# Performance work log

Measured on AMD Instinct MI355X. Metric: run time of the kernel, lower is better.

Reference implementation:

```python
import jax, jax.numpy as jnp
import numpy as np

BATCH = 32
N_LEVELS = (16384, 4096, 1024, 256)   # nodes at each mesh resolution
M_LEVELS = (4096, 1024, 256, 64)      # nodes after each Pool (downsample)
DEG = 6                               # directed edges per node
POOL_K = 3                            # nnz per row of downsample matrix
FILTERS = (3, 32, 32, 32, 64)         # channel chain of the 4 ChebConvs
K_CHEB = 6                            # Chebyshev polynomial order


def setup_inputs() -> dict:
    key = jax.random.key(0)
    ks = iter(jax.random.split(key, 64))
    inp = {"x": jax.random.normal(next(ks), (BATCH, N_LEVELS[0], FILTERS[0]), jnp.float32)}
    for i, N in enumerate(N_LEVELS):
        er = jnp.repeat(jnp.arange(N), DEG)
        off = jax.random.randint(next(ks), (N * DEG,), 1, N)
        inp[f"er{i}"] = er
        inp[f"ec{i}"] = (er + off) % N  # guaranteed no self loops
    for i, (M, N) in enumerate(zip(M_LEVELS, N_LEVELS)):
        inp[f"pr{i}"] = jnp.repeat(jnp.arange(M), POOL_K)
        inp[f"pc{i}"] = jax.random.randint(next(ks), (M * POOL_K,), 0, N)
        inp[f"pv{i}"] = jax.random.uniform(next(ks), (M * POOL_K,), jnp.float32)
    for i in range(4):
        fin, fout = FILTERS[i], FILTERS[i + 1]
        scale = 1.0 / np.sqrt(fin * K_CHEB)
        inp[f"W{i}"] = jax.random.normal(next(ks), (K_CHEB, fin, fout), jnp.float32) * scale
        inp[f"b{i}"] = jnp.zeros((fout,), jnp.float32)
    inp["enc_W"] = jax.random.normal(next(ks), (M_LEVELS[-1] * FILTERS[-1], 128), jnp.float32) * 0.1
    inp["enc_b"] = jnp.zeros((128,), jnp.float32)
    inp["cls_W"] = jax.random.normal(next(ks), (128, 10), jnp.float32) * 0.1
    inp["cls_b"] = jnp.zeros((10,), jnp.float32)
    return inp


def _cheb_conv(x, er, ec, W, b):
    # x: [B,N,Fin]; W: [K,Fin,Fout].
    # PyG ChebConv with lambda_max=2: L_hat = L - I = -D^{-1/2} A D^{-1/2}.
    N = x.shape[1]
    deg = jnp.zeros((N,), x.dtype).at[er].add(1.0)
    dinv = jnp.where(deg > 0, 1.0 / jnp.sqrt(jnp.maximum(deg, 1.0)), 0.0)
    norm = -(dinv[er] * dinv[ec])  # [E]

    def L(t):  # sparse matvec: gather neighbor feats, weight, scatter-add
        return jnp.zeros_like(t).at[:, er].add(t[:, ec] * norm[None, :, None])

    Tx0 = x
    out = jnp.einsum("bnf,fg->bng", Tx0, W[0])
    Tx1 = L(x)
    out = out + jnp.einsum("bnf,fg->bng", Tx1, W[1])
    for k in range(2, W.shape[0]):
        Tx2 = 2.0 * L(Tx1) - Tx0
        out = out + jnp.einsum("bnf,fg->bng", Tx2, W[k])
        Tx0, Tx1 = Tx1, Tx2
    return out + b


def _pool(x, pr, pc, pv, m):
    # sparse downsample matrix [m,N]: index_select cols * value, scatter_add rows
    B, _, F = x.shape
    return jnp.zeros((B, m, F), x.dtype).at[:, pr].add(x[:, pc] * pv[None, :, None])


def reference(x, er0, ec0, er1, ec1, er2, ec2, er3, ec3,
              pr0, pc0, pv0, pr1, pc1, pv1, pr2, pc2, pv2, pr3, pc3, pv3,
              W0, b0, W1, b1, W2, b2, W3, b3, enc_W, enc_b, cls_W, cls_b):
    ers, ecs = (er0, er1, er2, er3), (ec0, ec1, ec2, ec3)
    prs, pcs, pvs = (pr0, pr1, pr2, pr3), (pc0, pc1, pc2, pc3), (pv0, pv1, pv2, pv3)
    Ws, bs = (W0, W1, W2, W3), (b0, b1, b2, b3)
    for i in range(4):  # fixed n_layers loop (structurally distinct layers)
        x = jax.nn.relu(_cheb_conv(x, ers[i], ecs[i], Ws[i], bs[i]))
        x = _pool(x, prs[i], pcs[i], pvs[i], M_LEVELS[i])
    x = x.reshape(x.shape[0], -1)  # [B, 64*64]
    h = jax.nn.relu(x @ enc_W + enc_b)
    return h @ cls_W + cls_b
```

## Files before the change

kernel.cpp:

```cpp
#include <hip/hip_runtime.h>
#include <cstddef>
#include <cstdint>

#define BATCH 32


__device__ __forceinline__ void fma4(float4& a, float s, const float4& w) {
  a.x += s * w.x; a.y += s * w.y; a.z += s * w.z; a.w += s * w.w;
}
__device__ __forceinline__ float4 relu4(const float4& a) {
  return make_float4(fmaxf(a.x, 0.f), fmaxf(a.y, 0.f), fmaxf(a.z, 0.f), fmaxf(a.w, 0.f));
}

__global__ void __launch_bounds__(256) transpose_x(
    const float* __restrict__ x, float* __restrict__ xt)
{
  int t = blockIdx.x * 256 + threadIdx.x;
  int n = t / 96;
  int r = t % 96;
  int b = r / 3;
  int f = r - b * 3;
  xt[t] = x[((size_t)b * 16384 + n) * 3 + f];
}

template<int N, int R4>
__global__ void __launch_bounds__(256) cheb_step_nm(
    const float4* __restrict__ Tin, const float4* __restrict__ Tpp,
    const int* __restrict__ ec, float4* __restrict__ Tout,
    float coef, float beta)
{
  int idx = blockIdx.x * 256 + threadIdx.x;
  int n = idx / R4;
  int r = idx % R4;
  const int* e = ec + n * 6;
  float4 s = make_float4(0.f, 0.f, 0.f, 0.f);
#pragma unroll
  for (int d = 0; d < 6; ++d) {
    float4 v = Tin[(size_t)e[d] * R4 + r];
    s.x += v.x; s.y += v.y; s.z += v.z; s.w += v.w;
  }
  float4 p = Tpp[idx];
  float4 o;
  o.x = coef * s.x + beta * p.x;
  o.y = coef * s.y + beta * p.y;
  o.z = coef * s.z + beta * p.z;
  o.w = coef * s.w + beta * p.w;
  Tout[idx] = o;
}

template<int N, int F, int FS, int THREADS, int MINW>
__global__ void __launch_bounds__(THREADS, MINW) cheb_recur_reg(
    const float* __restrict__ X,
    const int* __restrict__ ec,
    float* __restrict__ T)
{
  constexpr int NPT = N / THREADS;
  __shared__ float cur[N * FS];
  const float cI = -1.0f / 6.0f;
  const float cS = -1.0f / 3.0f;
  const int b = blockIdx.x & 31;
  const int fbase = (blockIdx.x >> 5) * FS;
  constexpr size_t SL = (size_t)N * 32 * F;
  float prevv[NPT][FS];
  float curv[NPT][FS];
#pragma unroll
  for (int i = 0; i < NPT; ++i) {
    int n = threadIdx.x + i * THREADS;
    const float* src = X + ((size_t)n * 32 + b) * F + fbase;
#pragma unroll
    for (int f = 0; f < FS; ++f) { float v = src[f]; cur[n * FS + f] = v; curv[i][f] = v; }
  }
  __syncthreads();
#pragma unroll 1
  for (int k = 1; k <= 5; ++k) {
    float newv[NPT][FS];
    float* Tk = T + (size_t)(k - 1) * SL;
#pragma unroll
    for (int i = 0; i < NPT; ++i) {
      int n = threadIdx.x + i * THREADS;
      const int* e = ec + n * 6;
      float s[FS];
#pragma unroll
      for (int f = 0; f < FS; ++f) s[f] = 0.f;
#pragma unroll
      for (int d = 0; d < 6; ++d) {
        int c = e[d];
#pragma unroll
        for (int f = 0; f < FS; ++f) s[f] += cur[c * FS + f];
      }
      float* dst = Tk + ((size_t)n * 32 + b) * F + fbase;
#pragma unroll
      for (int f = 0; f < FS; ++f) {
        float v = (k == 1) ? (cI * s[f]) : (cS * s[f] - prevv[i][f]);
        newv[i][f] = v;
        dst[f] = v;
      }
    }
    __syncthreads();
#pragma unroll
    for (int i = 0; i < NPT; ++i) {
      int n = threadIdx.x + i * THREADS;
#pragma unroll
      for (int f = 0; f < FS; ++f) {
        prevv[i][f] = curv[i][f];
        curv[i][f] = newv[i][f];
        cur[n * FS + f] = newv[i][f];
      }
    }
    __syncthreads();
  }
}

template<int N, int M, int FOUT, bool OUT_BM>
__global__ void __launch_bounds__(256) pool_conv_f3(
    const float* __restrict__ X, const float* __restrict__ T,
    const float* __restrict__ W, const float* __restrict__ bias,
    const int* __restrict__ pc, const float* __restrict__ pv,
    float* __restrict__ out)
{
  constexpr int F4 = FOUT / 4;
  constexpr size_t SL = (size_t)N * BATCH * 3;
  __shared__ float Ws[6 * 3 * FOUT];
  for (int i = threadIdx.x; i < 6 * 3 * FOUT; i += 256) Ws[i] = W[i];
  __syncthreads();
  const float4* Ws4 = (const float4*)Ws;
  int t = blockIdx.x * 256 + threadIdx.x;
  int fo4 = t % F4;
  int b   = (t / F4) % BATCH;
  int m   = t / (F4 * BATCH);
  int c0 = pc[m * 3 + 0], c1 = pc[m * 3 + 1], c2 = pc[m * 3 + 2];
  float v0 = pv[m * 3 + 0], v1 = pv[m * 3 + 1], v2 = pv[m * 3 + 2];
  float4 bi = ((const float4*)bias)[fo4];
  float4 a0 = bi, a1 = bi, a2 = bi;
#pragma unroll
  for (int k = 0; k < 6; ++k) {
    const float* base = (k == 0) ? X : (T + (size_t)(k - 1) * SL);
    const float* r0 = base + ((size_t)c0 * BATCH + b) * 3;
    const float* r1 = base + ((size_t)c1 * BATCH + b) * 3;
    const float* r2 = base + ((size_t)c2 * BATCH + b) * 3;
#pragma unroll
    for (int f = 0; f < 3; ++f) {
      float4 w = Ws4[(k * 3 + f) * F4 + fo4];
      fma4(a0, r0[f], w);
      fma4(a1, r1[f], w);
      fma4(a2, r2[f], w);
    }
  }
  a0 = relu4(a0); a1 = relu4(a1); a2 = relu4(a2);
  float4 acc;
  acc.x = v0*a0.x + v1*a1.x + v2*a2.x;
  acc.y = v0*a0.y + v1*a1.y + v2*a2.y;
  acc.z = v0*a0.z + v1*a1.z + v2*a2.z;
  acc.w = v0*a0.w + v1*a1.w + v2*a2.w;
  size_t oi = OUT_BM ? (((size_t)b * M + m) * F4 + fo4) : (((size_t)m * BATCH + b) * F4 + fo4);
  ((float4*)out)[oi] = acc;
}

template<int N, int M, int FOUT, bool OUT_BM>
__global__ void __launch_bounds__(256) pool_conv_v32(
    const float* __restrict__ X, const float* __restrict__ T,
    const float* __restrict__ W, const float* __restrict__ bias,
    const int* __restrict__ pc, const float* __restrict__ pv,
    float* __restrict__ out)
{
  constexpr int FIN = 32;
  constexpr int F4 = FOUT / 4;
  constexpr size_t SL4 = (size_t)N * BATCH * FIN / 4;
  __shared__ float Ws[6 * FIN * FOUT];
  for (int i = threadIdx.x; i < 6 * FIN * FOUT; i += 256) Ws[i] = W[i];
  __syncthreads();
  const float4* Ws4 = (const float4*)Ws;
  const float4* X4p = (const float4*)X;
  const float4* T4s = (const float4*)T;
  int t = blockIdx.x * 256 + threadIdx.x;
  int fo4 = t % F4;
  int b   = (t / F4) % BATCH;
  int m   = t / (F4 * BATCH);
  int c0 = pc[m * 3 + 0], c1 = pc[m * 3 + 1], c2 = pc[m * 3 + 2];
  float v0 = pv[m * 3 + 0], v1 = pv[m * 3 + 1], v2 = pv[m * 3 + 2];
  float4 bi = ((const float4*)bias)[fo4];
  float4 a0 = bi, a1 = bi, a2 = bi;
#pragma unroll 1
  for (int k = 0; k < 6; ++k) {
    const float4* base = (k == 0) ? X4p : (T4s + (size_t)(k - 1) * SL4);
    const float4* r0 = base + ((size_t)c0 * BATCH + b) * 8;
    const float4* r1 = base + ((size_t)c1 * BATCH + b) * 8;
    const float4* r2 = base + ((size_t)c2 * BATCH + b) * 8;
#pragma unroll
    for (int fi = 0; fi < 8; ++fi) {
      float4 t0 = r0[fi], t1 = r1[fi], t2 = r2[fi];
#pragma unroll
      for (int ff = 0; ff < 4; ++ff) {
        float4 w = Ws4[((k * 32) + fi * 4 + ff) * F4 + fo4];
        fma4(a0, ((const float*)&t0)[ff], w);
        fma4(a1, ((const float*)&t1)[ff], w);
        fma4(a2, ((const float*)&t2)[ff], w);
      }
    }
  }
  a0 = relu4(a0); a1 = relu4(a1); a2 = relu4(a2);
  float4 acc;
  acc.x = v0*a0.x + v1*a1.x + v2*a2.x;
  acc.y = v0*a0.y + v1*a1.y + v2*a2.y;
  acc.z = v0*a0.z + v1*a1.z + v2*a2.z;
  acc.w = v0*a0.w + v1*a1.w + v2*a2.w;
  size_t oi = OUT_BM ? (((size_t)b * M + m) * F4 + fo4) : (((size_t)m * BATCH + b) * F4 + fo4);
  ((float4*)out)[oi] = acc;
}

__global__ void __launch_bounds__(256) encoder_partial(
    const float* __restrict__ Xf, const float* __restrict__ encW,
    float* __restrict__ partial)
{
  int b  = blockIdx.x;
  int ks = blockIdx.y;
  int fo = threadIdx.x & 127;
  int half = threadIdx.x >> 7;
  const float* xr = Xf + b * 4096 + ks * 256 + half * 128;
  const float* w  = encW + (size_t)(ks * 256 + half * 128) * 128;
  float acc = 0.f;
#pragma unroll 8
  for (int i = 0; i < 128; ++i) acc += xr[i] * w[(size_t)i * 128 + fo];
  __shared__ float part[256];
  part[threadIdx.x] = acc;
  __syncthreads();
  if (half == 0) partial[(size_t)(b * 16 + ks) * 128 + fo] = part[fo] + part[128 + fo];
}

__global__ void __launch_bounds__(128) encoder_reduce_cls(
    const float* __restrict__ partial, const float* __restrict__ encB,
    const float* __restrict__ clsW, const float* __restrict__ clsB,
    float* __restrict__ out)
{
  int b = blockIdx.x;
  int fo = threadIdx.x;
  float acc = encB[fo];
#pragma unroll
  for (int ks = 0; ks < 16; ++ks) acc += partial[(size_t)(b * 16 + ks) * 128 + fo];
  __shared__ float Hs[128];
  Hs[fo] = fmaxf(acc, 0.f);
  __syncthreads();
  if (fo < 10) {
    float s = clsB[fo];
#pragma unroll 4
    for (int f = 0; f < 128; ++f) s += Hs[f] * clsW[f * 10 + fo];
    out[b * 10 + fo] = s;
  }
}

extern "C" void kernel_launch(void* const* d_in, const int* in_sizes, int n_in,
                              void* d_out, int out_size, void* d_ws, size_t ws_size,
                              hipStream_t stream)
{
  const float* x   = (const float*)d_in[0];
  const int* ec0 = (const int*)d_in[2];
  const int* ec1 = (const int*)d_in[4];
  const int* ec2 = (const int*)d_in[6];
  const int* ec3 = (const int*)d_in[8];
  const int* pc0 = (const int*)d_in[10]; const float* pv0 = (const float*)d_in[11];
  const int* pc1 = (const int*)d_in[13]; const float* pv1 = (const float*)d_in[14];
  const int* pc2 = (const int*)d_in[16]; const float* pv2 = (const float*)d_in[17];
  const int* pc3 = (const int*)d_in[19]; const float* pv3 = (const float*)d_in[20];
  const float* W0 = (const float*)d_in[21]; const float* b0 = (const float*)d_in[22];
  const float* W1 = (const float*)d_in[23]; const float* b1 = (const float*)d_in[24];
  const float* W2 = (const float*)d_in[25]; const float* b2 = (const float*)d_in[26];
  const float* W3 = (const float*)d_in[27]; const float* b3 = (const float*)d_in[28];
  const float* encW = (const float*)d_in[29]; const float* encB = (const float*)d_in[30];
  const float* clsW = (const float*)d_in[31]; const float* clsB = (const float*)d_in[32];
  float* out = (float*)d_out;

  float* ws = (float*)d_ws;
  float* Xt = ws;
  float* T  = Xt + 1572864;
  float* X1 = T  + 20971520;
  float* X2 = X1 + 4194304;
  float* X3 = X2 + 1048576;
  float* X4 = X3 + 262144;
  float* P  = X4 + 131072;

  const float cI = -1.0f / 6.0f;
  const float cS = -1.0f / 3.0f;
  dim3 blk(256);

  transpose_x<<<dim3(6144), blk, 0, stream>>>(x, Xt);

  {
    constexpr size_t S = (size_t)16384 * 96;
    const float4* Xt4 = (const float4*)Xt;
    cheb_step_nm<16384, 24><<<dim3(1536), blk, 0, stream>>>(
        Xt4, Xt4, ec0, (float4*)T, cI, 0.f);
    cheb_step_nm<16384, 24><<<dim3(1536), blk, 0, stream>>>(
        (const float4*)T, Xt4, ec0, (float4*)(T + S), cS, -1.f);
    cheb_step_nm<16384, 24><<<dim3(1536), blk, 0, stream>>>(
        (const float4*)(T + S), (const float4*)T, ec0, (float4*)(T + 2 * S), cS, -1.f);
    cheb_step_nm<16384, 24><<<dim3(1536), blk, 0, stream>>>(
        (const float4*)(T + 2 * S), (const float4*)(T + S), ec0, (float4*)(T + 3 * S), cS, -1.f);
    cheb_step_nm<16384, 24><<<dim3(1536), blk, 0, stream>>>(
        (const float4*)(T + 3 * S), (const float4*)(T + 2 * S), ec0, (float4*)(T + 4 * S), cS, -1.f);
    pool_conv_f3<16384, 4096, 32, false><<<dim3(4096), blk, 0, stream>>>(
        Xt, T, W0, b0, pc0, pv0, X1);
  }
  {
    cheb_recur_reg<4096, 32, 2, 1024, 8><<<dim3(512), dim3(1024), 0, stream>>>(X1, ec1, T);
    pool_conv_v32<4096, 1024, 32, false><<<dim3(1024), blk, 0, stream>>>(
        X1, T, W1, b1, pc1, pv1, X2);
  }
  {
    cheb_recur_reg<1024, 32, 2, 256, 8><<<dim3(512), blk, 0, stream>>>(X2, ec2, T);
    pool_conv_v32<1024, 256, 32, false><<<dim3(256), blk, 0, stream>>>(
        X2, T, W2, b2, pc2, pv2, X3);
  }
  {
    cheb_recur_reg<256, 32, 2, 256, 8><<<dim3(512), blk, 0, stream>>>(X3, ec3, T);
    pool_conv_v32<256, 64, 64, true><<<dim3(128), blk, 0, stream>>>(
        X3, T, W3, b3, pc3, pv3, X4);
  }
  encoder_partial<<<dim3(32, 16), blk, 0, stream>>>(X4, encW, P);
  encoder_reduce_cls<<<dim3(32), dim3(128), 0, stream>>>(P, encB, clsW, clsB, out);
}
```

Before: 327.3 us.

## Store Chebyshev terms slab-major so recurrence writes coalesce, adapt pool gather

```diff
diff --git a/kernel.cpp b/kernel.cpp
--- a/kernel.cpp
+++ b/kernel.cpp
@@ -48,64 +48,59 @@
   Tout[idx] = o;
 }
 
-template<int N, int F, int FS, int THREADS, int MINW>
-__global__ void __launch_bounds__(THREADS, MINW) cheb_recur_reg(
+template<int N, int F, int THREADS, int MINW>
+__global__ void __launch_bounds__(THREADS, MINW) cheb_recur_sm(
     const float* __restrict__ X,
     const int* __restrict__ ec,
     float* __restrict__ T)
 {
+  constexpr int FS = 2;
   constexpr int NPT = N / THREADS;
   __shared__ float cur[N * FS];
   const float cI = -1.0f / 6.0f;
   const float cS = -1.0f / 3.0f;
   const int b = blockIdx.x & 31;
-  const int fbase = (blockIdx.x >> 5) * FS;
+  const int slab = blockIdx.x >> 5;
+  const int fbase = slab * FS;
   constexpr size_t SL = (size_t)N * 32 * F;
   float prevv[NPT][FS];
-  float curv[NPT][FS];
 #pragma unroll
   for (int i = 0; i < NPT; ++i) {
     int n = threadIdx.x + i * THREADS;
-    const float* src = X + ((size_t)n * 32 + b) * F + fbase;
-#pragma unroll
-    for (int f = 0; f < FS; ++f) { float v = src[f]; cur[n * FS + f] = v; curv[i][f] = v; }
+    float2 v = *(const float2*)(X + ((size_t)n * 32 + b) * F + fbase);
+    cur[n * FS + 0] = v.x;
+    cur[n * FS + 1] = v.y;
   }
   __syncthreads();
 #pragma unroll 1
   for (int k = 1; k <= 5; ++k) {
     float newv[NPT][FS];
-    float* Tk = T + (size_t)(k - 1) * SL;
+    float2* Tk = (float2*)(T + (size_t)(k - 1) * SL) + (size_t)(slab * 32 + b) * N;
 #pragma unroll
     for (int i = 0; i < NPT; ++i) {
       int n = threadIdx.x + i * THREADS;
       const int* e = ec + n * 6;
-      float s[FS];
-#pragma unroll
-      for (int f = 0; f < FS; ++f) s[f] = 0.f;
+      float s0 = 0.f, s1 = 0.f;
 #pragma unroll
       for (int d = 0; d < 6; ++d) {
         int c = e[d];
-#pragma unroll
-        for (int f = 0; f < FS; ++f) s[f] += cur[c * FS + f];
+        s0 += cur[c * FS + 0];
+        s1 += cur[c * FS + 1];
       }
-      float* dst = Tk + ((size_t)n * 32 + b) * F + fbase;
-#pragma unroll
-      for (int f = 0; f < FS; ++f) {
-        float v = (k == 1) ? (cI * s[f]) : (cS * s[f] - prevv[i][f]);
-        newv[i][f] = v;
-        dst[f] = v;
-      }
+      float v0, v1;
+      if (k == 1) { v0 = cI * s0; v1 = cI * s1; }
+      else        { v0 = cS * s0 - prevv[i][0]; v1 = cS * s1 - prevv[i][1]; }
+      newv[i][0] = v0; newv[i][1] = v1;
+      Tk[n] = make_float2(v0, v1);
     }
     __syncthreads();
 #pragma unroll
     for (int i = 0; i < NPT; ++i) {
       int n = threadIdx.x + i * THREADS;
-#pragma unroll
-      for (int f = 0; f < FS; ++f) {
-        prevv[i][f] = curv[i][f];
-        curv[i][f] = newv[i][f];
-        cur[n * FS + f] = newv[i][f];
-      }
+      prevv[i][0] = cur[n * FS + 0];
+      prevv[i][1] = cur[n * FS + 1];
+      cur[n * FS + 0] = newv[i][0];
+      cur[n * FS + 1] = newv[i][1];
     }
     __syncthreads();
   }
@@ -157,21 +152,20 @@
 }
 
 template<int N, int M, int FOUT, bool OUT_BM>
-__global__ void __launch_bounds__(256) pool_conv_v32(
-    const float* __restrict__ X, const float* __restrict__ T,
+__global__ void __launch_bounds__(256) pool_conv_sm(
+    const float* __restrict__ X,
+    const float* __restrict__ T,
     const float* __restrict__ W, const float* __restrict__ bias,
     const int* __restrict__ pc, const float* __restrict__ pv,
     float* __restrict__ out)
 {
-  constexpr int FIN = 32;
   constexpr int F4 = FOUT / 4;
-  constexpr size_t SL4 = (size_t)N * BATCH * FIN / 4;
-  __shared__ float Ws[6 * FIN * FOUT];
-  for (int i = threadIdx.x; i < 6 * FIN * FOUT; i += 256) Ws[i] = W[i];
+  constexpr size_t SL = (size_t)N * BATCH * 32;
+  __shared__ float Ws[6 * 32 * FOUT];
+  for (int i = threadIdx.x; i < 6 * 32 * FOUT; i += 256) Ws[i] = W[i];
   __syncthreads();
   const float4* Ws4 = (const float4*)Ws;
   const float4* X4p = (const float4*)X;
-  const float4* T4s = (const float4*)T;
   int t = blockIdx.x * 256 + threadIdx.x;
   int fo4 = t % F4;
   int b   = (t / F4) % BATCH;
@@ -180,22 +174,36 @@
   float v0 = pv[m * 3 + 0], v1 = pv[m * 3 + 1], v2 = pv[m * 3 + 2];
   float4 bi = ((const float4*)bias)[fo4];
   float4 a0 = bi, a1 = bi, a2 = bi;
-#pragma unroll 1
-  for (int k = 0; k < 6; ++k) {
-    const float4* base = (k == 0) ? X4p : (T4s + (size_t)(k - 1) * SL4);
-    const float4* r0 = base + ((size_t)c0 * BATCH + b) * 8;
-    const float4* r1 = base + ((size_t)c1 * BATCH + b) * 8;
-    const float4* r2 = base + ((size_t)c2 * BATCH + b) * 8;
+  {
+    const float4* r0 = X4p + ((size_t)c0 * BATCH + b) * 8;
+    const float4* r1 = X4p + ((size_t)c1 * BATCH + b) * 8;
+    const float4* r2 = X4p + ((size_t)c2 * BATCH + b) * 8;
 #pragma unroll
     for (int fi = 0; fi < 8; ++fi) {
       float4 t0 = r0[fi], t1 = r1[fi], t2 = r2[fi];
 #pragma unroll
       for (int ff = 0; ff < 4; ++ff) {
-        float4 w = Ws4[((k * 32) + fi * 4 + ff) * F4 + fo4];
+        float4 w = Ws4[(fi * 4 + ff) * F4 + fo4];
         fma4(a0, ((const float*)&t0)[ff], w);
         fma4(a1, ((const float*)&t1)[ff], w);
         fma4(a2, ((const float*)&t2)[ff], w);
       }
+    }
+  }
+#pragma unroll 1
+  for (int k = 1; k < 6; ++k) {
+    const float2* Tk = (const float2*)(T + (size_t)(k - 1) * SL);
+#pragma unroll
+    for (int s = 0; s < 16; ++s) {
+      size_t sb = (size_t)(s * 32 + b) * N;
+      float2 t0 = Tk[sb + c0];
+      float2 t1 = Tk[sb + c1];
+      float2 t2 = Tk[sb + c2];
+      float4 w0 = Ws4[(k * 32 + s * 2 + 0) * F4 + fo4];
+      float4 w1 = Ws4[(k * 32 + s * 2 + 1) * F4 + fo4];
+      fma4(a0, t0.x, w0); fma4(a0, t0.y, w1);
+      fma4(a1, t1.x, w0); fma4(a1, t1.y, w1);
+      fma4(a2, t2.x, w0); fma4(a2, t2.y, w1);
     }
   }
   a0 = relu4(a0); a1 = relu4(a1); a2 = relu4(a2);
@@ -301,18 +309,18 @@
         Xt, T, W0, b0, pc0, pv0, X1);
   }
   {
-    cheb_recur_reg<4096, 32, 2, 1024, 8><<<dim3(512), dim3(1024), 0, stream>>>(X1, ec1, T);
-    pool_conv_v32<4096, 1024, 32, false><<<dim3(1024), blk, 0, stream>>>(
+    cheb_recur_sm<4096, 32, 512, 4><<<dim3(512), dim3(512), 0, stream>>>(X1, ec1, T);
+    pool_conv_sm<4096, 1024, 32, false><<<dim3(1024), blk, 0, stream>>>(
         X1, T, W1, b1, pc1, pv1, X2);
   }
   {
-    cheb_recur_reg<1024, 32, 2, 256, 8><<<dim3(512), blk, 0, stream>>>(X2, ec2, T);
-    pool_conv_v32<1024, 256, 32, false><<<dim3(256), blk, 0, stream>>>(
+    cheb_recur_sm<1024, 32, 256, 4><<<dim3(512), blk, 0, stream>>>(X2, ec2, T);
+    pool_conv_sm<1024, 256, 32, false><<<dim3(256), blk, 0, stream>>>(
         X2, T, W2, b2, pc2, pv2, X3);
   }
   {
-    cheb_recur_reg<256, 32, 2, 256, 8><<<dim3(512), blk, 0, stream>>>(X3, ec3, T);
-    pool_conv_v32<256, 64, 64, true><<<dim3(128), blk, 0, stream>>>(
+    cheb_recur_sm<256, 32, 256, 4><<<dim3(512), blk, 0, stream>>>(X3, ec3, T);
+    pool_conv_sm<256, 64, 64, true><<<dim3(128), blk, 0, stream>>>(
         X3, T, W3, b3, pc3, pv3, X4);
   }
   encoder_partial<<<dim3(32, 16), blk, 0, stream>>>(X4, encW, P);
```

Measured after the change: 393.9 us. +20.3%, slower.
